# Kernel optimization log

Hardware: AMD Instinct MI355X
Metric: run time of the kernel (lower is better)

## Reference

```python
import jax, jax.numpy as jnp
import numpy as np

N = 50000      # nodes
E = 800000     # edges
F = 128        # num_node_features
H = 128        # hidden_dim
DEPTH = 4
G = 512        # number of graphs in batch
BN_EPS = 1e-5


def setup_inputs() -> dict:
    key = jax.random.key(0)
    ks = jax.random.split(key, 10)
    x = jax.random.normal(ks[0], (N, F), dtype=jnp.float32)
    edge_index = jax.random.randint(ks[1], (2, E), 0, N, dtype=jnp.int64)
    batch = jnp.sort(jax.random.randint(ks[2], (N,), 0, G, dtype=jnp.int64))
    W_emb = jax.random.normal(ks[3], (F, H), dtype=jnp.float32) / np.sqrt(F)
    b_emb = jnp.zeros((H,), dtype=jnp.float32)
    W_conv = jax.random.normal(ks[4], (DEPTH, H, H), dtype=jnp.float32) / np.sqrt(H)
    b_conv = jnp.zeros((DEPTH, H), dtype=jnp.float32)
    gamma = jnp.ones((DEPTH - 1, H), dtype=jnp.float32)
    beta = jnp.zeros((DEPTH - 1, H), dtype=jnp.float32)
    return {"x": x, "edge_index": edge_index, "batch": batch,
            "W_emb": W_emb, "b_emb": b_emb, "W_conv": W_conv,
            "b_conv": b_conv, "gamma": gamma, "beta": beta}


def _gcn_conv(h, W, b, src, dst, dinv):
    # PyG GCNConv: D^{-1/2}(A+I)D^{-1/2} (h W) + b, with self-loops folded in
    hw = h @ W  # [N, H]
    norm = dinv[src] * dinv[dst]  # [E]
    agg = jax.ops.segment_sum(norm[:, None] * hw[src], dst, num_segments=N)
    agg = agg + (dinv * dinv)[:, None] * hw  # self-loop contribution
    return agg + b


def _batchnorm(h, g, b):
    mu = jnp.mean(h, axis=0)
    var = jnp.var(h, axis=0)
    return (h - mu) * jax.lax.rsqrt(var + BN_EPS) * g + b


def reference(x, edge_index, batch, W_emb, b_emb, W_conv, b_conv, gamma, beta):
    src, dst = edge_index[0], edge_index[1]
    # degrees incl. self-loop for symmetric GCN normalization
    deg = jax.ops.segment_sum(jnp.ones((E,), jnp.float32), dst, num_segments=N) + 1.0
    dinv = jax.lax.rsqrt(deg)
    h = x @ W_emb + b_emb  # embedding Linear
    for i in range(DEPTH):
        h = _gcn_conv(h, W_conv[i], b_conv[i], src, dst, dinv)
        if i < DEPTH - 1:
            h = jax.nn.relu(h)
            h = _batchnorm(h, gamma[i], beta[i])
    # global mean pool over graph ids
    counts = jax.ops.segment_sum(jnp.ones((N,), jnp.float32), batch, num_segments=G)
    pooled = jax.ops.segment_sum(h, batch, num_segments=G)
    return pooled / jnp.maximum(counts, 1.0)[:, None]
```

## Files before the change

### kernel.cpp

```cpp
#include <hip/hip_runtime.h>
#include <hip/hip_fp16.h>
#include <math.h>

#define HDIM 128
#define BKT_SHIFT 7
#define NBMAX 512
#define CHUNK 4096
#define NBS 512

typedef __attribute__((ext_vector_type(8))) short bf16x8;
typedef __attribute__((ext_vector_type(4))) float f32x4;

union U4 { unsigned int u[4]; bf16x8 v; };

__device__ __forceinline__ unsigned int cvt_pk_bf16(float a, float b) {
    unsigned int r;
    asm("v_cvt_pk_bf16_f32 %0, %1, %2" : "=v"(r) : "v"(a), "v"(b));
    return r;
}

__device__ __forceinline__ void split8(const float* v, bf16x8& ah, bf16x8& al) {
    U4 H, L;
    #pragma unroll
    for (int p = 0; p < 4; p++) {
        unsigned int h = cvt_pk_bf16(v[2 * p], v[2 * p + 1]);
        H.u[p] = h;
        float h0 = __uint_as_float(h << 16);
        float h1 = __uint_as_float(h & 0xFFFF0000u);
        L.u[p] = cvt_pk_bf16(v[2 * p] - h0, v[2 * p + 1] - h1);
    }
    ah = H.v; al = L.v;
}

__global__ __launch_bounds__(256) void bucket_hist(const int* __restrict__ dst,
                                                   int* __restrict__ bcount, int E) {
    __shared__ int h[NBMAX];
    int t = threadIdx.x;
    for (int b = t; b < NBMAX; b += 256) h[b] = 0;
    __syncthreads();
    int i = blockIdx.x * blockDim.x + t;
    int stride = gridDim.x * blockDim.x;
    for (; i < E; i += stride) atomicAdd(&h[dst[i] >> BKT_SHIFT], 1);
    __syncthreads();
    for (int b = t; b < NBMAX; b += 256) {
        int c = h[b];
        if (c) atomicAdd(&bcount[b], c);
    }
}

__global__ __launch_bounds__(256) void bucket_scan(const int* __restrict__ bcount,
                                                   int* __restrict__ bases,
                                                   int* __restrict__ cursor, int E) {
    int t = threadIdx.x;
    int v0 = bcount[2 * t], v1 = bcount[2 * t + 1];
    int s = v0 + v1;
    __shared__ int ss[256];
    ss[t] = s; __syncthreads();
    #pragma unroll
    for (int off = 1; off < 256; off <<= 1) {
        int u = (t >= off) ? ss[t - off] : 0;
        __syncthreads();
        ss[t] += u;
        __syncthreads();
    }
    int ex = ss[t] - s;
    bases[2 * t] = ex;          cursor[2 * t] = ex;
    bases[2 * t + 1] = ex + v0; cursor[2 * t + 1] = ex + v0;
    if (t == 255) bases[NBMAX] = E;
}

__global__ __launch_bounds__(256) void bucket_scatter(const int* __restrict__ src,
                                                      const int* __restrict__ dst,
                                                      int* __restrict__ cursor,
                                                      unsigned* __restrict__ ebuf, int E) {
    __shared__ unsigned sbuf[CHUNK];
    __shared__ int hist[NBMAX], hbase[NBMAX], gbase[NBMAX], cnt2[NBMAX];
    __shared__ int ss[256];
    int t = threadIdx.x;
    int start = blockIdx.x * CHUNK;
    int n = min(CHUNK, E - start);

    for (int b = t; b < NBMAX; b += 256) { hist[b] = 0; cnt2[b] = 0; }
    __syncthreads();
    for (int i = t; i < n; i += 256) atomicAdd(&hist[dst[start + i] >> BKT_SHIFT], 1);
    __syncthreads();

    int v0 = hist[2 * t], v1 = hist[2 * t + 1];
    int s = v0 + v1;
    ss[t] = s; __syncthreads();
    #pragma unroll
    for (int off = 1; off < 256; off <<= 1) {
        int u = (t >= off) ? ss[t - off] : 0;
        __syncthreads();
        ss[t] += u;
        __syncthreads();
    }
    int ex = ss[t] - s;
    hbase[2 * t] = ex;
    hbase[2 * t + 1] = ex + v0;
    if (v0 > 0) gbase[2 * t] = atomicAdd(&cursor[2 * t], v0);
    if (v1 > 0) gbase[2 * t + 1] = atomicAdd(&cursor[2 * t + 1], v1);
    __syncthreads();

    for (int i = t; i < n; i += 256) {
        int d = dst[start + i];
        int bkt = d >> BKT_SHIFT;
        unsigned p = ((unsigned)(d & 127) << 24) | (unsigned)src[start + i];
        int pos = atomicAdd(&cnt2[bkt], 1);
        sbuf[hbase[bkt] + pos] = p;
    }
    __syncthreads();

    for (int b = t; b < NBMAX; b += 256) {
        int c = hist[b], hb = hbase[b], gb = gbase[b];
        for (int j = 0; j < c; j++) ebuf[gb + j] = sbuf[hb + j];
    }
}

__global__ __launch_bounds__(256) void bucket_finalize(const unsigned* __restrict__ ebuf,
                                                       const int* __restrict__ bases,
                                                       int* __restrict__ csr,
                                                       int* __restrict__ offs,
                                                       float* __restrict__ dinv,
                                                       int N, int E) {
    int b = blockIdx.x;
    int beg = bases[b], end = bases[b + 1];
    __shared__ int hist[128], pre[128], cnt2[128];
    int t = threadIdx.x;
    if (t < 128) { hist[t] = 0; cnt2[t] = 0; }
    __syncthreads();
    for (int i = beg + t; i < end; i += 256)
        atomicAdd(&hist[(ebuf[i] >> 24) & 127], 1);
    __syncthreads();
    if (t < 128) pre[t] = hist[t];
    __syncthreads();
    #pragma unroll
    for (int off = 1; off < 128; off <<= 1) {
        int v = (t < 128 && t >= off) ? pre[t - off] : 0;
        __syncthreads();
        if (t < 128) pre[t] += v;
        __syncthreads();
    }
    if (t < 128) {
        int node = b * 128 + t;
        if (node < N) {
            int ex = pre[t] - hist[t];
            offs[node] = beg + ex;
            dinv[node] = rsqrtf((float)hist[t] + 1.0f);
        }
    }
    if (b == 0 && t == 0) offs[N] = E;
    __syncthreads();
    for (int i = beg + t; i < end; i += 256) {
        unsigned p = ebuf[i];
        int dl = (p >> 24) & 127;
        int pos = atomicAdd(&cnt2[dl], 1);
        csr[beg + (pre[dl] - hist[dl]) + pos] = (int)(p & 0xFFFFFFu);
    }
}

__global__ void wsplit_all(const float* __restrict__ W_emb, const float* __restrict__ W_conv,
                           short* __restrict__ wt) {
    int gid = blockIdx.x * 256 + threadIdx.x;
    if (gid >= 5 * 16384) return;
    int m = gid >> 14;
    int i = gid & 16383;
    int n = i >> 7, k = i & 127;
    const float* src = (m == 0) ? W_emb : (W_conv + (size_t)(m - 1) * 16384);
    float v = src[k * 128 + n];
    unsigned int u = __float_as_uint(v);
    unsigned int hi = (u + 0x7FFFu + ((u >> 16) & 1)) & 0xFFFF0000u;
    float hf = __uint_as_float(hi);
    float lo = v - hf;
    unsigned int ul = __float_as_uint(lo);
    unsigned int lo16 = (ul + 0x7FFFu + ((ul >> 16) & 1)) >> 16;
    short* Whi = wt + (size_t)m * 32768;
    Whi[i] = (short)(hi >> 16);
    Whi[16384 + i] = (short)lo16;
}

template <bool OUT_F16>
__global__ __launch_bounds__(256) void gemm_mfma(const float* __restrict__ A,
                                                 const short* __restrict__ Wh,
                                                 const short* __restrict__ Wl,
                                                 const float* __restrict__ aff_s,
                                                 const float* __restrict__ aff_t,
                                                 const float* __restrict__ bias,
                                                 const float* __restrict__ rowscale,
                                                 void* __restrict__ outp, int N) {
    int w = threadIdx.x >> 6;
    int lane = threadIdx.x & 63;
    int l15 = lane & 15, lg = lane >> 4;
    int r0 = blockIdx.x * 128 + (w >> 1) * 64;
    int c0 = (w & 1) * 64;

    f32x4 acc[4][4];
    #pragma unroll
    for (int tc = 0; tc < 4; tc++) {
        float bz = bias ? bias[c0 + tc * 16 + l15] : 0.0f;
        #pragma unroll
        for (int tr = 0; tr < 4; tr++) {
            acc[tr][tc][0] = bz; acc[tr][tc][1] = bz;
            acc[tr][tc][2] = bz; acc[tr][tc][3] = bz;
        }
    }

    #pragma unroll
    for (int kt = 0; kt < 4; kt++) {
        int kk = kt * 32 + lg * 8;

        bf16x8 bh[4], bl[4];
        #pragma unroll
        for (int tc = 0; tc < 4; tc++) {
            int n = c0 + tc * 16 + l15;
            bh[tc] = *(const bf16x8*)(Wh + n * 128 + kk);
            bl[tc] = *(const bf16x8*)(Wl + n * 128 + kk);
        }

        float sv[8], tv[8];
        if (aff_s) {
            *(float4*)&sv[0] = *(const float4*)(aff_s + kk);
            *(float4*)&sv[4] = *(const float4*)(aff_s + kk + 4);
            *(float4*)&tv[0] = *(const float4*)(aff_t + kk);
            *(float4*)&tv[4] = *(const float4*)(aff_t + kk + 4);
        }

        bf16x8 ah[4], al[4];
        #pragma unroll
        for (int tr = 0; tr < 4; tr++) {
            int row = min(r0 + tr * 16 + l15, N - 1);
            const float* ap = A + (size_t)row * 128 + kk;
            float v[8];
            *(float4*)&v[0] = *(const float4*)ap;
            *(float4*)&v[4] = *(const float4*)(ap + 4);
            if (aff_s) {
                #pragma unroll
                for (int j = 0; j < 8; j++) v[j] = fmaf(v[j], sv[j], tv[j]);
            }
            split8(v, ah[tr], al[tr]);
        }

        #pragma unroll
        for (int tr = 0; tr < 4; tr++) {
            #pragma unroll
            for (int tc = 0; tc < 4; tc++) {
                acc[tr][tc] = __builtin_amdgcn_mfma_f32_16x16x32_bf16(ah[tr], bh[tc], acc[tr][tc], 0, 0, 0);
                acc[tr][tc] = __builtin_amdgcn_mfma_f32_16x16x32_bf16(ah[tr], bl[tc], acc[tr][tc], 0, 0, 0);
                acc[tr][tc] = __builtin_amdgcn_mfma_f32_16x16x32_bf16(al[tr], bh[tc], acc[tr][tc], 0, 0, 0);
            }
        }
    }

    #pragma unroll
    for (int tr = 0; tr < 4; tr++) {
        #pragma unroll
        for (int r = 0; r < 4; r++) {
            int row = r0 + tr * 16 + lg * 4 + r;
            if (row < N) {
                float sc = rowscale ? rowscale[row] : 1.0f;
                #pragma unroll
                for (int tc = 0; tc < 4; tc++) {
                    int col = c0 + tc * 16 + l15;
                    float val = acc[tr][tc][r] * sc;
                    if (OUT_F16) {
                        ((__half*)outp)[(size_t)row * 128 + col] = __float2half(val);
                    } else {
                        ((float*)outp)[(size_t)row * 128 + col] = val;
                    }
                }
            }
        }
    }
}

__global__ __launch_bounds__(256) void gather_kernel(const __half* __restrict__ hws,
                                                     const int* __restrict__ csr_src,
                                                     const int* __restrict__ offs,
                                                     const float* __restrict__ dinv,
                                                     const float* __restrict__ bias,
                                                     float* __restrict__ out,
                                                     int N, int relu) {
    int lane = threadIdx.x & 63;
    int q = lane >> 4;
    int sq = lane & 15;
    int node = blockIdx.x * 4 + (threadIdx.x >> 6);
    if (node >= N) return;
    int lo = offs[node], hi = offs[node + 1];

    const uint4* base = (const uint4*)hws;
    float4 a0 = make_float4(0.f, 0.f, 0.f, 0.f), a1 = a0;

    #define ACCUM_U4(u)  do {                                                    \
        float2 p0 = __half22float2(*(__half2*)&(u).x);                           \
        float2 p1 = __half22float2(*(__half2*)&(u).y);                           \
        float2 p2 = __half22float2(*(__half2*)&(u).z);                           \
        float2 p3 = __half22float2(*(__half2*)&(u).w);                           \
        a0.x += p0.x; a0.y += p0.y; a0.z += p1.x; a0.w += p1.y;                  \
        a1.x += p2.x; a1.y += p2.y; a1.z += p3.x; a1.w += p3.y;                  \
    } while (0)

    int j = lo + q;
    for (; j + 12 < hi; j += 16) {
        int s0 = csr_src[j], s1 = csr_src[j + 4], s2 = csr_src[j + 8], s3 = csr_src[j + 12];
        uint4 u0 = base[(size_t)s0 * 16 + sq];
        uint4 u1 = base[(size_t)s1 * 16 + sq];
        uint4 u2 = base[(size_t)s2 * 16 + sq];
        uint4 u3 = base[(size_t)s3 * 16 + sq];
        ACCUM_U4(u0); ACCUM_U4(u1); ACCUM_U4(u2); ACCUM_U4(u3);
    }
    for (; j < hi; j += 4) {
        int s = csr_src[j];
        uint4 u = base[(size_t)s * 16 + sq];
        ACCUM_U4(u);
    }
    if (q == 0) {
        uint4 u = base[(size_t)node * 16 + sq];
        ACCUM_U4(u);
    }
    #undef ACCUM_U4

    a0.x += __shfl_xor(a0.x, 16); a0.y += __shfl_xor(a0.y, 16);
    a0.z += __shfl_xor(a0.z, 16); a0.w += __shfl_xor(a0.w, 16);
    a1.x += __shfl_xor(a1.x, 16); a1.y += __shfl_xor(a1.y, 16);
    a1.z += __shfl_xor(a1.z, 16); a1.w += __shfl_xor(a1.w, 16);
    a0.x += __shfl_xor(a0.x, 32); a0.y += __shfl_xor(a0.y, 32);
    a0.z += __shfl_xor(a0.z, 32); a0.w += __shfl_xor(a0.w, 32);
    a1.x += __shfl_xor(a1.x, 32); a1.y += __shfl_xor(a1.y, 32);
    a1.z += __shfl_xor(a1.z, 32); a1.w += __shfl_xor(a1.w, 32);

    if (q == 0) {
        float di = dinv[node];
        float4 b0 = ((const float4*)bias)[2 * sq];
        float4 b1 = ((const float4*)bias)[2 * sq + 1];
        float4 o0, o1;
        o0.x = di * a0.x + b0.x; o0.y = di * a0.y + b0.y;
        o0.z = di * a0.z + b0.z; o0.w = di * a0.w + b0.w;
        o1.x = di * a1.x + b1.x; o1.y = di * a1.y + b1.y;
        o1.z = di * a1.z + b1.z; o1.w = di * a1.w + b1.w;
        if (relu) {
            o0.x = fmaxf(o0.x, 0.f); o0.y = fmaxf(o0.y, 0.f);
            o0.z = fmaxf(o0.z, 0.f); o0.w = fmaxf(o0.w, 0.f);
            o1.x = fmaxf(o1.x, 0.f); o1.y = fmaxf(o1.y, 0.f);
            o1.z = fmaxf(o1.z, 0.f); o1.w = fmaxf(o1.w, 0.f);
        }
        ((float4*)(out + (size_t)node * HDIM))[2 * sq] = o0;
        ((float4*)(out + (size_t)node * HDIM))[2 * sq + 1] = o1;
    }
}

__global__ __launch_bounds__(256) void bn_stats_p(const float* __restrict__ h,
                                                  float* __restrict__ Psum,
                                                  float* __restrict__ Qsum, int N) {
    int sl = threadIdx.x & 31;
    int rg = threadIdx.x >> 5;
    float4 s = make_float4(0.f, 0.f, 0.f, 0.f), q = s;
    const int S = NBS * 8;
    for (int n = blockIdx.x * 8 + rg; n < N; n += 4 * S) {
        int n1 = n + S, n2 = n + 2 * S, n3 = n + 3 * S;
        float4 v0 = ((const float4*)(h + (size_t)n * HDIM))[sl];
        float4 v1 = (n1 < N) ? ((const float4*)(h + (size_t)n1 * HDIM))[sl] : make_float4(0.f, 0.f, 0.f, 0.f);
        float4 v2 = (n2 < N) ? ((const float4*)(h + (size_t)n2 * HDIM))[sl] : make_float4(0.f, 0.f, 0.f, 0.f);
        float4 v3 = (n3 < N) ? ((const float4*)(h + (size_t)n3 * HDIM))[sl] : make_float4(0.f, 0.f, 0.f, 0.f);
        s.x += v0.x + v1.x + v2.x + v3.x;
        s.y += v0.y + v1.y + v2.y + v3.y;
        s.z += v0.z + v1.z + v2.z + v3.z;
        s.w += v0.w + v1.w + v2.w + v3.w;
        q.x += v0.x * v0.x + v1.x * v1.x + v2.x * v2.x + v3.x * v3.x;
        q.y += v0.y * v0.y + v1.y * v1.y + v2.y * v2.y + v3.y * v3.y;
        q.z += v0.z * v0.z + v1.z * v1.z + v2.z * v2.z + v3.z * v3.z;
        q.w += v0.w * v0.w + v1.w * v1.w + v2.w * v2.w + v3.w * v3.w;
    }
    __shared__ float4 rs[256], rq[256];
    rs[threadIdx.x] = s; rq[threadIdx.x] = q;
    __syncthreads();
    #pragma unroll
    for (int off = 4; off >= 1; off >>= 1) {
        if (rg < off) {
            float4 os = rs[threadIdx.x + off * 32], oq = rq[threadIdx.x + off * 32];
            s.x += os.x; s.y += os.y; s.z += os.z; s.w += os.w;
            q.x += oq.x; q.y += oq.y; q.z += oq.z; q.w += oq.w;
            rs[threadIdx.x] = s; rq[threadIdx.x] = q;
        }
        __syncthreads();
    }
    if (rg == 0) {
        size_t base = (size_t)blockIdx.x * HDIM;
        ((float4*)(Psum + base))[sl] = s;
        ((float4*)(Qsum + base))[sl] = q;
    }
}

__global__ __launch_bounds__(256) void bn_finalize_p(const float* __restrict__ Psum,
                                                     const float* __restrict__ Qsum,
                                                     const float* __restrict__ gamma,
                                                     const float* __restrict__ beta,
                                                     float* __restrict__ aff_s,
                                                     float* __restrict__ aff_t,
                                                     int N, int nblk) {
    int t = threadIdx.x;
    int total4 = nblk * 32;
    float4 s = make_float4(0.f, 0.f, 0.f, 0.f), q = s;
    for (int i = t; i < total4; i += 256) {
        float4 p = ((const float4*)Psum)[i];
        float4 r = ((const float4*)Qsum)[i];
        s.x += p.x; s.y += p.y; s.z += p.z; s.w += p.w;
        q.x += r.x; q.y += r.y; q.z += r.z; q.w += r.w;
    }
    __shared__ float4 rs[256], rq[256];
    rs[t] = s; rq[t] = q;
    __syncthreads();
    int fq = t & 31;
    int rg = t >> 5;
    #pragma unroll
    for (int off = 4; off >= 1; off >>= 1) {
        if (rg < off) {
            float4 os = rs[t + off * 32], oq = rq[t + off * 32];
            s.x += os.x; s.y += os.y; s.z += os.z; s.w += os.w;
            q.x += oq.x; q.y += oq.y; q.z += oq.z; q.w += oq.w;
            rs[t] = s; rq[t] = q;
        }
        __syncthreads();
    }
    if (rg == 0) {
        float inv = 1.0f / (float)N;
        float sv[4] = { s.x, s.y, s.z, s.w };
        float qv[4] = { q.x, q.y, q.z, q.w };
        #pragma unroll
        for (int j = 0; j < 4; j++) {
            int f = 4 * fq + j;
            float m = sv[j] * inv;
            float var = qv[j] * inv - m * m;
            float sc = gamma[f] * rsqrtf(var + 1e-5f);
            aff_s[f] = sc;
            aff_t[f] = beta[f] - m * sc;
        }
    }
}

__device__ __forceinline__ int lower_bound_i(const int* __restrict__ arr, int n, int val) {
    int lo = 0, hi = n;
    while (lo < hi) {
        int mid = (lo + hi) >> 1;
        if (arr[mid] < val) lo = mid + 1; else hi = mid;
    }
    return lo;
}

__global__ __launch_bounds__(256) void pool_kernel(const float* __restrict__ h,
                                                   const int* __restrict__ batch,
                                                   float* __restrict__ out, int N, int G) {
    int g = blockIdx.x;
    int lo = lower_bound_i(batch, N, g);
    int hi = lower_bound_i(batch, N, g + 1);
    int sl = threadIdx.x & 31;
    int rg = threadIdx.x >> 5;

    float4 acc = make_float4(0.f, 0.f, 0.f, 0.f);
    for (int n = lo + rg; n < hi; n += 8) {
        float4 v = ((const float4*)(h + (size_t)n * HDIM))[sl];
        acc.x += v.x; acc.y += v.y; acc.z += v.z; acc.w += v.w;
    }

    __shared__ float4 red[256];
    red[threadIdx.x] = acc;
    __syncthreads();
    if (rg < 4) {
        float4 o = red[threadIdx.x + 128];
        acc.x += o.x; acc.y += o.y; acc.z += o.z; acc.w += o.w;
        red[threadIdx.x] = acc;
    }
    __syncthreads();
    if (rg < 2) {
        float4 o = red[threadIdx.x + 64];
        acc.x += o.x; acc.y += o.y; acc.z += o.z; acc.w += o.w;
        red[threadIdx.x] = acc;
    }
    __syncthreads();
    if (rg == 0) {
        float4 o = red[threadIdx.x + 32];
        float inv = 1.0f / fmaxf((float)(hi - lo), 1.0f);
        float4 r;
        r.x = (acc.x + o.x) * inv;
        r.y = (acc.y + o.y) * inv;
        r.z = (acc.z + o.z) * inv;
        r.w = (acc.w + o.w) * inv;
        ((float4*)(out + (size_t)g * HDIM))[sl] = r;
    }
}

extern "C" void kernel_launch(void* const* d_in, const int* in_sizes, int n_in,
                              void* d_out, int out_size, void* d_ws, size_t ws_size,
                              hipStream_t stream) {
    const float* x      = (const float*)d_in[0];
    const int*   ei     = (const int*)d_in[1];
    const int*   batch  = (const int*)d_in[2];
    const float* W_emb  = (const float*)d_in[3];
    const float* b_emb  = (const float*)d_in[4];
    const float* W_conv = (const float*)d_in[5];
    const float* b_conv = (const float*)d_in[6];
    const float* gamma  = (const float*)d_in[7];
    const float* beta   = (const float*)d_in[8];

    const int E = in_sizes[1] / 2;
    const int N = in_sizes[2];
    const int G = out_size / HDIM;
    const int DEPTH = 4;

    const int* srcp = ei;
    const int* dstp = ei + E;
    float* out = (float*)d_out;

    size_t NH = (size_t)N * HDIM;
    size_t npad = ((size_t)N + 63) & ~(size_t)63;
    size_t epad = ((size_t)E + 63) & ~(size_t)63;
    int nb = (N + 127) / 128;

    float* ws = (float*)d_ws;
    float* dinv    = ws;
    int*   offs    = (int*)(dinv + npad);
    int*   bases   = offs + npad + 64;
    int*   cursor  = bases + 1024;
    int*   bcount  = cursor + NBMAX;
    int*   csr     = bcount + NBMAX;
    unsigned* ebuf = (unsigned*)(csr + epad);
    float* Psum    = (float*)(ebuf + epad);
    float* Qsum    = Psum + NBS * HDIM;
    float* aff_s   = Qsum + NBS * HDIM;
    float* aff_t   = aff_s + 128;
    short* wt      = (short*)(aff_t + 128);
    float* hbuf    = (float*)(wt + 5 * 2 * 16384);
    __half* hws16  = (__half*)(hbuf + NH);

    wsplit_all<<<(5 * 16384 + 255) / 256, 256, 0, stream>>>(W_emb, W_conv, wt);

    hipMemsetAsync(bcount, 0, NBMAX * sizeof(int), stream);
    bucket_hist<<<256, 256, 0, stream>>>(dstp, bcount, E);
    bucket_scan<<<1, 256, 0, stream>>>(bcount, bases, cursor, E);
    bucket_scatter<<<(E + CHUNK - 1) / CHUNK, 256, 0, stream>>>(srcp, dstp, cursor, ebuf, E);
    bucket_finalize<<<nb, 256, 0, stream>>>(ebuf, bases, csr, offs, dinv, N, E);

    int gemm_blocks = (N + 127) / 128;
    int gather_blocks = (N + 3) / 4;

    gemm_mfma<false><<<gemm_blocks, 256, 0, stream>>>(x, wt, wt + 16384, nullptr, nullptr,
                                                      b_emb, nullptr, hbuf, N);

    for (int l = 0; l < DEPTH; l++) {
        short* whi = wt + (size_t)(l + 1) * 32768;
        gemm_mfma<true><<<gemm_blocks, 256, 0, stream>>>(hbuf, whi, whi + 16384,
                                                         (l > 0) ? aff_s : nullptr,
                                                         (l > 0) ? aff_t : nullptr,
                                                         nullptr, dinv, hws16, N);
        gather_kernel<<<gather_blocks, 256, 0, stream>>>(hws16, csr, offs, dinv,
                                                         b_conv + (size_t)l * HDIM, hbuf,
                                                         N, (l < DEPTH - 1) ? 1 : 0);
        if (l < DEPTH - 1) {
            bn_stats_p<<<NBS, 256, 0, stream>>>(hbuf, Psum, Qsum, N);
            bn_finalize_p<<<1, 256, 0, stream>>>(Psum, Qsum, gamma + (size_t)l * HDIM,
                                                 beta + (size_t)l * HDIM, aff_s, aff_t,
                                                 N, NBS);
        }
    }

    pool_kernel<<<G, 256, 0, stream>>>(hbuf, batch, out, N, G);
}
```

Before: 387.1 us.

## Fuse BatchNorm statistics into gather kernel and add two-stage partial reduction

```diff
diff --git a/kernel.cpp b/kernel.cpp
--- a/kernel.cpp
+++ b/kernel.cpp
@@ -6,7 +6,7 @@
 #define BKT_SHIFT 7
 #define NBMAX 512
 #define CHUNK 4096
-#define NBS 512
+#define NRED 512
 
 typedef __attribute__((ext_vector_type(8))) short bf16x8;
 typedef __attribute__((ext_vector_type(4))) float f32x4;
@@ -273,121 +273,125 @@
     }
 }
 
+template <bool BN>
 __global__ __launch_bounds__(256) void gather_kernel(const __half* __restrict__ hws,
                                                      const int* __restrict__ csr_src,
                                                      const int* __restrict__ offs,
                                                      const float* __restrict__ dinv,
                                                      const float* __restrict__ bias,
                                                      float* __restrict__ out,
-                                                     int N, int relu) {
+                                                     float* __restrict__ Psum,
+                                                     float* __restrict__ Qsum,
+                                                     int N) {
+    __shared__ float sP[4][128], sQ[4][128];
     int lane = threadIdx.x & 63;
     int q = lane >> 4;
     int sq = lane & 15;
-    int node = blockIdx.x * 4 + (threadIdx.x >> 6);
-    if (node >= N) return;
-    int lo = offs[node], hi = offs[node + 1];
-
-    const uint4* base = (const uint4*)hws;
-    float4 a0 = make_float4(0.f, 0.f, 0.f, 0.f), a1 = a0;
-
-    #define ACCUM_U4(u)  do {                                                    \
-        float2 p0 = __half22float2(*(__half2*)&(u).x);                           \
-        float2 p1 = __half22float2(*(__half2*)&(u).y);                           \
-        float2 p2 = __half22float2(*(__half2*)&(u).z);                           \
-        float2 p3 = __half22float2(*(__half2*)&(u).w);                           \
-        a0.x += p0.x; a0.y += p0.y; a0.z += p1.x; a0.w += p1.y;                  \
-        a1.x += p2.x; a1.y += p2.y; a1.z += p3.x; a1.w += p3.y;                  \
-    } while (0)
-
-    int j = lo + q;
-    for (; j + 12 < hi; j += 16) {
-        int s0 = csr_src[j], s1 = csr_src[j + 4], s2 = csr_src[j + 8], s3 = csr_src[j + 12];
-        uint4 u0 = base[(size_t)s0 * 16 + sq];
-        uint4 u1 = base[(size_t)s1 * 16 + sq];
-        uint4 u2 = base[(size_t)s2 * 16 + sq];
-        uint4 u3 = base[(size_t)s3 * 16 + sq];
-        ACCUM_U4(u0); ACCUM_U4(u1); ACCUM_U4(u2); ACCUM_U4(u3);
-    }
-    for (; j < hi; j += 4) {
-        int s = csr_src[j];
-        uint4 u = base[(size_t)s * 16 + sq];
-        ACCUM_U4(u);
-    }
-    if (q == 0) {
-        uint4 u = base[(size_t)node * 16 + sq];
-        ACCUM_U4(u);
-    }
-    #undef ACCUM_U4
-
-    a0.x += __shfl_xor(a0.x, 16); a0.y += __shfl_xor(a0.y, 16);
-    a0.z += __shfl_xor(a0.z, 16); a0.w += __shfl_xor(a0.w, 16);
-    a1.x += __shfl_xor(a1.x, 16); a1.y += __shfl_xor(a1.y, 16);
-    a1.z += __shfl_xor(a1.z, 16); a1.w += __shfl_xor(a1.w, 16);
-    a0.x += __shfl_xor(a0.x, 32); a0.y += __shfl_xor(a0.y, 32);
-    a0.z += __shfl_xor(a0.z, 32); a0.w += __shfl_xor(a0.w, 32);
-    a1.x += __shfl_xor(a1.x, 32); a1.y += __shfl_xor(a1.y, 32);
-    a1.z += __shfl_xor(a1.z, 32); a1.w += __shfl_xor(a1.w, 32);
-
-    if (q == 0) {
-        float di = dinv[node];
-        float4 b0 = ((const float4*)bias)[2 * sq];
-        float4 b1 = ((const float4*)bias)[2 * sq + 1];
-        float4 o0, o1;
-        o0.x = di * a0.x + b0.x; o0.y = di * a0.y + b0.y;
-        o0.z = di * a0.z + b0.z; o0.w = di * a0.w + b0.w;
-        o1.x = di * a1.x + b1.x; o1.y = di * a1.y + b1.y;
-        o1.z = di * a1.z + b1.z; o1.w = di * a1.w + b1.w;
-        if (relu) {
-            o0.x = fmaxf(o0.x, 0.f); o0.y = fmaxf(o0.y, 0.f);
-            o0.z = fmaxf(o0.z, 0.f); o0.w = fmaxf(o0.w, 0.f);
-            o1.x = fmaxf(o1.x, 0.f); o1.y = fmaxf(o1.y, 0.f);
-            o1.z = fmaxf(o1.z, 0.f); o1.w = fmaxf(o1.w, 0.f);
-        }
-        ((float4*)(out + (size_t)node * HDIM))[2 * sq] = o0;
-        ((float4*)(out + (size_t)node * HDIM))[2 * sq + 1] = o1;
-    }
-}
-
-__global__ __launch_bounds__(256) void bn_stats_p(const float* __restrict__ h,
-                                                  float* __restrict__ Psum,
-                                                  float* __restrict__ Qsum, int N) {
-    int sl = threadIdx.x & 31;
-    int rg = threadIdx.x >> 5;
-    float4 s = make_float4(0.f, 0.f, 0.f, 0.f), q = s;
-    const int S = NBS * 8;
-    for (int n = blockIdx.x * 8 + rg; n < N; n += 4 * S) {
-        int n1 = n + S, n2 = n + 2 * S, n3 = n + 3 * S;
-        float4 v0 = ((const float4*)(h + (size_t)n * HDIM))[sl];
-        float4 v1 = (n1 < N) ? ((const float4*)(h + (size_t)n1 * HDIM))[sl] : make_float4(0.f, 0.f, 0.f, 0.f);
-        float4 v2 = (n2 < N) ? ((const float4*)(h + (size_t)n2 * HDIM))[sl] : make_float4(0.f, 0.f, 0.f, 0.f);
-        float4 v3 = (n3 < N) ? ((const float4*)(h + (size_t)n3 * HDIM))[sl] : make_float4(0.f, 0.f, 0.f, 0.f);
-        s.x += v0.x + v1.x + v2.x + v3.x;
-        s.y += v0.y + v1.y + v2.y + v3.y;
-        s.z += v0.z + v1.z + v2.z + v3.z;
-        s.w += v0.w + v1.w + v2.w + v3.w;
-        q.x += v0.x * v0.x + v1.x * v1.x + v2.x * v2.x + v3.x * v3.x;
-        q.y += v0.y * v0.y + v1.y * v1.y + v2.y * v2.y + v3.y * v3.y;
-        q.z += v0.z * v0.z + v1.z * v1.z + v2.z * v2.z + v3.z * v3.z;
-        q.w += v0.w * v0.w + v1.w * v1.w + v2.w * v2.w + v3.w * v3.w;
-    }
-    __shared__ float4 rs[256], rq[256];
-    rs[threadIdx.x] = s; rq[threadIdx.x] = q;
-    __syncthreads();
-    #pragma unroll
-    for (int off = 4; off >= 1; off >>= 1) {
-        if (rg < off) {
-            float4 os = rs[threadIdx.x + off * 32], oq = rq[threadIdx.x + off * 32];
-            s.x += os.x; s.y += os.y; s.z += os.z; s.w += os.w;
-            q.x += oq.x; q.y += oq.y; q.z += oq.z; q.w += oq.w;
-            rs[threadIdx.x] = s; rq[threadIdx.x] = q;
-        }
-        __syncthreads();
-    }
-    if (rg == 0) {
-        size_t base = (size_t)blockIdx.x * HDIM;
-        ((float4*)(Psum + base))[sl] = s;
-        ((float4*)(Qsum + base))[sl] = q;
-    }
+    int wv = threadIdx.x >> 6;
+    int node = blockIdx.x * 4 + wv;
+    if (!BN && node >= N) return;
+
+    if (BN && q == 0) {
+        #pragma unroll
+        for (int j = 0; j < 8; j++) { sP[wv][8 * sq + j] = 0.f; sQ[wv][8 * sq + j] = 0.f; }
+    }
+
+    if (node < N) {
+        int lo = offs[node], hi = offs[node + 1];
+        const uint4* base = (const uint4*)hws;
+        float4 a0 = make_float4(0.f, 0.f, 0.f, 0.f), a1 = a0;
+
+        #define ACCUM_U4(u)  do {                                                    \
+            float2 p0 = __half22float2(*(__half2*)&(u).x);                           \
+            float2 p1 = __half22float2(*(__half2*)&(u).y);                           \
+            float2 p2 = __half22float2(*(__half2*)&(u).z);                           \
+            float2 p3 = __half22float2(*(__half2*)&(u).w);                           \
+            a0.x += p0.x; a0.y += p0.y; a0.z += p1.x; a0.w += p1.y;                  \
+            a1.x += p2.x; a1.y += p2.y; a1.z += p3.x; a1.w += p3.y;                  \
+        } while (0)
+
+        int j = lo + q;
+        for (; j + 12 < hi; j += 16) {
+            int s0 = csr_src[j], s1 = csr_src[j + 4], s2 = csr_src[j + 8], s3 = csr_src[j + 12];
+            uint4 u0 = base[(size_t)s0 * 16 + sq];
+            uint4 u1 = base[(size_t)s1 * 16 + sq];
+            uint4 u2 = base[(size_t)s2 * 16 + sq];
+            uint4 u3 = base[(size_t)s3 * 16 + sq];
+            ACCUM_U4(u0); ACCUM_U4(u1); ACCUM_U4(u2); ACCUM_U4(u3);
+        }
+        for (; j < hi; j += 4) {
+            int s = csr_src[j];
+            uint4 u = base[(size_t)s * 16 + sq];
+            ACCUM_U4(u);
+        }
+        if (q == 0) {
+            uint4 u = base[(size_t)node * 16 + sq];
+            ACCUM_U4(u);
+        }
+        #undef ACCUM_U4
+
+        a0.x += __shfl_xor(a0.x, 16); a0.y += __shfl_xor(a0.y, 16);
+        a0.z += __shfl_xor(a0.z, 16); a0.w += __shfl_xor(a0.w, 16);
+        a1.x += __shfl_xor(a1.x, 16); a1.y += __shfl_xor(a1.y, 16);
+        a1.z += __shfl_xor(a1.z, 16); a1.w += __shfl_xor(a1.w, 16);
+        a0.x += __shfl_xor(a0.x, 32); a0.y += __shfl_xor(a0.y, 32);
+        a0.z += __shfl_xor(a0.z, 32); a0.w += __shfl_xor(a0.w, 32);
+        a1.x += __shfl_xor(a1.x, 32); a1.y += __shfl_xor(a1.y, 32);
+        a1.z += __shfl_xor(a1.z, 32); a1.w += __shfl_xor(a1.w, 32);
+
+        if (q == 0) {
+            float di = dinv[node];
+            float4 b0 = ((const float4*)bias)[2 * sq];
+            float4 b1 = ((const float4*)bias)[2 * sq + 1];
+            float4 o0, o1;
+            o0.x = di * a0.x + b0.x; o0.y = di * a0.y + b0.y;
+            o0.z = di * a0.z + b0.z; o0.w = di * a0.w + b0.w;
+            o1.x = di * a1.x + b1.x; o1.y = di * a1.y + b1.y;
+            o1.z = di * a1.z + b1.z; o1.w = di * a1.w + b1.w;
+            if (BN) {
+                o0.x = fmaxf(o0.x, 0.f); o0.y = fmaxf(o0.y, 0.f);
+                o0.z = fmaxf(o0.z, 0.f); o0.w = fmaxf(o0.w, 0.f);
+                o1.x = fmaxf(o1.x, 0.f); o1.y = fmaxf(o1.y, 0.f);
+                o1.z = fmaxf(o1.z, 0.f); o1.w = fmaxf(o1.w, 0.f);
+                int f = 8 * sq;
+                sP[wv][f + 0] = o0.x; sQ[wv][f + 0] = o0.x * o0.x;
+                sP[wv][f + 1] = o0.y; sQ[wv][f + 1] = o0.y * o0.y;
+                sP[wv][f + 2] = o0.z; sQ[wv][f + 2] = o0.z * o0.z;
+                sP[wv][f + 3] = o0.w; sQ[wv][f + 3] = o0.w * o0.w;
+                sP[wv][f + 4] = o1.x; sQ[wv][f + 4] = o1.x * o1.x;
+                sP[wv][f + 5] = o1.y; sQ[wv][f + 5] = o1.y * o1.y;
+                sP[wv][f + 6] = o1.z; sQ[wv][f + 6] = o1.z * o1.z;
+                sP[wv][f + 7] = o1.w; sQ[wv][f + 7] = o1.w * o1.w;
+            }
+            ((float4*)(out + (size_t)node * HDIM))[2 * sq] = o0;
+            ((float4*)(out + (size_t)node * HDIM))[2 * sq + 1] = o1;
+        }
+    }
+
+    if (BN) {
+        __syncthreads();
+        int t = threadIdx.x;
+        if (t < 128) {
+            float p = sP[0][t] + sP[1][t] + sP[2][t] + sP[3][t];
+            float qq = sQ[0][t] + sQ[1][t] + sQ[2][t] + sQ[3][t];
+            Psum[(size_t)blockIdx.x * HDIM + t] = p;
+            Qsum[(size_t)blockIdx.x * HDIM + t] = qq;
+        }
+    }
+}
+
+__global__ __launch_bounds__(256) void bn_reduce(const float* __restrict__ Pin,
+                                                 const float* __restrict__ Qin,
+                                                 float* __restrict__ Pout,
+                                                 float* __restrict__ Qout, int nrows) {
+    int t = threadIdx.x;
+    int f = t & 127, h = t >> 7;
+    const float* src = h ? Qin : Pin;
+    float acc = 0.f;
+    for (int r = blockIdx.x; r < nrows; r += gridDim.x)
+        acc += src[(size_t)r * HDIM + f];
+    float* dst = h ? Qout : Pout;
+    dst[(size_t)blockIdx.x * HDIM + f] = acc;
 }
 
 __global__ __launch_bounds__(256) void bn_finalize_p(const float* __restrict__ Psum,
@@ -514,6 +518,7 @@
     size_t npad = ((size_t)N + 63) & ~(size_t)63;
     size_t epad = ((size_t)E + 63) & ~(size_t)63;
     int nb = (N + 127) / 128;
+    int gather_blocks = (N + 3) / 4;
 
     float* ws = (float*)d_ws;
     float* dinv    = ws;
@@ -524,8 +529,10 @@
     int*   csr     = bcount + NBMAX;
     unsigned* ebuf = (unsigned*)(csr + epad);
     float* Psum    = (float*)(ebuf + epad);
-    float* Qsum    = Psum + NBS * HDIM;
-    float* aff_s   = Qsum + NBS * HDIM;
+    float* Qsum    = Psum + (size_t)gather_blocks * HDIM;
+    float* Pred    = Qsum + (size_t)gather_blocks * HDIM;
+    float* Qred    = Pred + NRED * HDIM;
+    float* aff_s   = Qred + NRED * HDIM;
     float* aff_t   = aff_s + 128;
     short* wt      = (short*)(aff_t + 128);
     float* hbuf    = (float*)(wt + 5 * 2 * 16384);
@@ -540,7 +547,6 @@
     bucket_finalize<<<nb, 256, 0, stream>>>(ebuf, bases, csr, offs, dinv, N, E);
 
     int gemm_blocks = (N + 127) / 128;
-    int gather_blocks = (N + 3) / 4;
 
     gemm_mfma<false><<<gemm_blocks, 256, 0, stream>>>(x, wt, wt + 16384, nullptr, nullptr,
                                                       b_emb, nullptr, hbuf, N);
@@ -551,14 +557,18 @@
                                                          (l > 0) ? aff_s : nullptr,
                                                          (l > 0) ? aff_t : nullptr,
                                                          nullptr, dinv, hws16, N);
-        gather_kernel<<<gather_blocks, 256, 0, stream>>>(hws16, csr, offs, dinv,
-                                                         b_conv + (size_t)l * HDIM, hbuf,
-                                                         N, (l < DEPTH - 1) ? 1 : 0);
         if (l < DEPTH - 1) {
-            bn_stats_p<<<NBS, 256, 0, stream>>>(hbuf, Psum, Qsum, N);
-            bn_finalize_p<<<1, 256, 0, stream>>>(Psum, Qsum, gamma + (size_t)l * HDIM,
+            gather_kernel<true><<<gather_blocks, 256, 0, stream>>>(hws16, csr, offs, dinv,
+                                                                   b_conv + (size_t)l * HDIM,
+                                                                   hbuf, Psum, Qsum, N);
+            bn_reduce<<<NRED, 256, 0, stream>>>(Psum, Qsum, Pred, Qred, gather_blocks);
+            bn_finalize_p<<<1, 256, 0, stream>>>(Pred, Qred, gamma + (size_t)l * HDIM,
                                                  beta + (size_t)l * HDIM, aff_s, aff_t,
-                                                 N, NBS);
+                                                 N, NRED);
+        } else {
+            gather_kernel<false><<<gather_blocks, 256, 0, stream>>>(hws16, csr, offs, dinv,
+                                                                    b_conv + (size_t)l * HDIM,
+                                                                    hbuf, nullptr, nullptr, N);
         }
     }
 
```

After: 421.7 us. 8.9% more time.
